# Performance work log

Measured on AMD Instinct MI355X. Metric: run time of the kernel, lower is better.

Reference implementation:

```python
import jax, jax.numpy as jnp
import numpy as np

B, C, H, W = 4, 64, 64, 64
C8 = C // 8

def setup_inputs() -> dict:
    key = jax.random.key(0)
    ks = jax.random.split(key, 7)
    s = 0.05
    x  = jax.random.normal(ks[0], (B, C, H, W), dtype=jnp.float32)
    wq = jax.random.normal(ks[1], (C8, C), dtype=jnp.float32) * s
    bq = jax.random.normal(ks[2], (C8,), dtype=jnp.float32) * s
    wk = jax.random.normal(ks[3], (C8, C), dtype=jnp.float32) * s
    bk = jax.random.normal(ks[4], (C8,), dtype=jnp.float32) * s
    wv = jax.random.normal(ks[5], (C, C), dtype=jnp.float32) * s
    bv = jax.random.normal(ks[6], (C,), dtype=jnp.float32) * s
    return {"x": x, "wq": wq, "bq": bq, "wk": wk, "bk": bk, "wv": wv, "bv": bv}

def reference(x, wq, bq, wk, bk, wv, bv):
    b, c, h, w = x.shape
    n = h * w
    xf = x.reshape(b, c, n)                                   # [B,C,N]
    q = jnp.einsum('oc,bcn->bon', wq, xf) + bq[None, :, None]  # [B,C8,N]
    k = jnp.einsum('oc,bcn->bon', wk, xf) + bk[None, :, None]  # [B,C8,N]
    v = jnp.einsum('oc,bcn->bon', wv, xf) + bv[None, :, None]  # [B,C, N]
    scores = jnp.einsum('bci,bcj->bij', q, k)                  # [B,N,N]
    attn = jax.nn.softmax(scores, axis=-1)
    out = jnp.einsum('bcn,bnm->bcm', v, attn)                  # V @ A, as torch.bmm(value, attention)
    return out.reshape(b, c, h, w) + x
```

## Files before the change

### kernel.cpp

```cpp
#include <hip/hip_runtime.h>
#include <hip/hip_bf16.h>
#include <math.h>

#define NN 4096
#define CC 64

typedef float  f32x16 __attribute__((ext_vector_type(16)));
typedef short  bf16x8 __attribute__((ext_vector_type(8)));
typedef short  s16x4  __attribute__((ext_vector_type(4)));
typedef unsigned int u32x4 __attribute__((ext_vector_type(4)));

static __device__ __forceinline__ unsigned short f2bfu(float f) {
    __hip_bfloat16 h = __float2bfloat16(f);
    unsigned short s;
    __builtin_memcpy(&s, &h, 2);
    return s;
}
static __device__ __forceinline__ unsigned packbf(float lo, float hi) {
    return (unsigned)f2bfu(lo) | ((unsigned)f2bfu(hi) << 16);
}
static __device__ __forceinline__ f32x16 fzero16() {
    f32x16 z;
#pragma unroll
    for (int i = 0; i < 16; ++i) z[i] = 0.f;
    return z;
}
static __device__ __forceinline__ bf16x8 bzero8() {
    bf16x8 z;
#pragma unroll
    for (int i = 0; i < 8; ++i) z[i] = 0;
    return z;
}

static __device__ __forceinline__ void process_phalf(
        const f32x16& s, int hi,
        bf16x8 a0, bf16x8 a1, bf16x8 a2, bf16x8 a3,
        f32x16& accX, f32x16& accY) {
    unsigned g0 = packbf(__expf(s[0]),  __expf(s[1]));
    unsigned g1 = packbf(__expf(s[2]),  __expf(s[3]));
    unsigned g2 = packbf(__expf(s[4]),  __expf(s[5]));
    unsigned g3 = packbf(__expf(s[6]),  __expf(s[7]));
    unsigned g4 = packbf(__expf(s[8]),  __expf(s[9]));
    unsigned g5 = packbf(__expf(s[10]), __expf(s[11]));
    unsigned g6 = packbf(__expf(s[12]), __expf(s[13]));
    unsigned g7 = packbf(__expf(s[14]), __expf(s[15]));
    unsigned r0 = (unsigned)__shfl_xor((int)(hi ? g0 : g2), 32);
    unsigned r1 = (unsigned)__shfl_xor((int)(hi ? g1 : g3), 32);
    unsigned r2 = (unsigned)__shfl_xor((int)(hi ? g4 : g6), 32);
    unsigned r3 = (unsigned)__shfl_xor((int)(hi ? g5 : g7), 32);
    u32x4 b0u, b1u;
    b0u[0] = hi ? r0 : g0;  b0u[1] = hi ? r1 : g1;
    b0u[2] = hi ? g2 : r0;  b0u[3] = hi ? g3 : r1;
    b1u[0] = hi ? r2 : g4;  b1u[1] = hi ? r3 : g5;
    b1u[2] = hi ? g6 : r2;  b1u[3] = hi ? g7 : r3;
    bf16x8 bf0 = __builtin_bit_cast(bf16x8, b0u);
    bf16x8 bf1 = __builtin_bit_cast(bf16x8, b1u);
    accX = __builtin_amdgcn_mfma_f32_32x32x16_bf16(a0, bf0, accX, 0, 0, 0);
    accX = __builtin_amdgcn_mfma_f32_32x32x16_bf16(a1, bf1, accX, 0, 0, 0);
    accY = __builtin_amdgcn_mfma_f32_32x32x16_bf16(a2, bf0, accY, 0, 0, 0);
    accY = __builtin_amdgcn_mfma_f32_32x32x16_bf16(a3, bf1, accY, 0, 0, 0);
}

__global__ __launch_bounds__(256) void proj_all(
        const float* __restrict__ x,
        const float* __restrict__ wq, const float* __restrict__ bq,
        const float* __restrict__ wk, const float* __restrict__ bk,
        const float* __restrict__ wv, const float* __restrict__ bv,
        short* __restrict__ qb, short* __restrict__ kb, float* __restrict__ vT) {
    int t = threadIdx.x;
    int w = t >> 6, ml = t & 31, hi = (t >> 5) & 1;
    int rt = blockIdx.x >> 7;
    int nt = (blockIdx.x & 127) * 4 + w;
    int ng = nt * 32 + ml;
    int b = ng >> 12, nb_ = ng & 4095;
    const float* xc = x + ((size_t)b * CC) * NN + nb_;

    int rg = 32 * rt + ml;
    const float* wrow =
        rg < 8  ? wq + (size_t)rg * 64 :
        rg < 16 ? wk + (size_t)(rg - 8) * 64 :
        rg < 80 ? wv + (size_t)(rg - 16) * 64 : wq;
    bool wvalid = (rg < 80);

    f32x16 acc = fzero16();
#pragma unroll
    for (int s = 0; s < 4; ++s) {
        int c0 = 16 * s + 8 * hi;
        float xv[8];
#pragma unroll
        for (int j = 0; j < 8; ++j) xv[j] = xc[(size_t)(c0 + j) * NN];
        u32x4 xg;
#pragma unroll
        for (int j = 0; j < 4; ++j) xg[j] = packbf(xv[2 * j], xv[2 * j + 1]);
        bf16x8 xf = __builtin_bit_cast(bf16x8, xg);

        bf16x8 af;
        if (wvalid) {
            float4 f0 = *(const float4*)(wrow + c0);
            float4 f1 = *(const float4*)(wrow + c0 + 4);
            u32x4 ag;
            ag[0] = packbf(f0.x, f0.y); ag[1] = packbf(f0.z, f0.w);
            ag[2] = packbf(f1.x, f1.y); ag[3] = packbf(f1.z, f1.w);
            af = __builtin_bit_cast(bf16x8, ag);
        } else {
            af = bzero8();
        }
        acc = __builtin_amdgcn_mfma_f32_32x32x16_bf16(af, xf, acc, 0, 0, 0);
    }

    if (rt == 0) {
        s16x4 qv, kv;
#pragma unroll
        for (int j = 0; j < 4; ++j) {
            qv[j] = (short)f2bfu(acc[j] + bq[j + 4 * hi]);
            kv[j] = (short)f2bfu(acc[j + 4] + bk[j + 4 * hi]);
        }
        *(s16x4*)(qb + (size_t)ng * 8 + 4 * hi) = qv;
        *(s16x4*)(kb + (size_t)ng * 8 + 4 * hi) = kv;
#pragma unroll
        for (int r = 8; r < 16; ++r) {
            int rowr = (r & 3) + 8 * (r >> 2) + 4 * hi;
            int c = rowr - 16;
            vT[((size_t)(b * CC + c)) * NN + nb_] = acc[r] + bv[c];
        }
    } else if (rt == 1) {
#pragma unroll
        for (int r = 0; r < 16; ++r) {
            int rowr = (r & 3) + 8 * (r >> 2) + 4 * hi;
            int c = rowr + 16;
            vT[((size_t)(b * CC + c)) * NN + nb_] = acc[r] + bv[c];
        }
    } else {
#pragma unroll
        for (int r = 0; r < 8; ++r) {
            int rowr = (r & 3) + 8 * (r >> 2) + 4 * hi;
            int c = rowr + 48;
            vT[((size_t)(b * CC + c)) * NN + nb_] = acc[r] + bv[c];
        }
    }
}

__global__ __launch_bounds__(512) void stats_mfma(
        const short* __restrict__ qb, const short* __restrict__ kb,
        const float* __restrict__ vT, short* __restrict__ vsT) {
    int b = blockIdx.x >> 7;
    int nbase = (blockIdx.x & 127) * 32;
    int t = threadIdx.x;
    int w = __builtin_amdgcn_readfirstlane(t >> 6);
    int ml = t & 31, hi = (t >> 5) & 1;

    bf16x8 qf = bzero8();
    if (!hi) qf = *(const bf16x8*)(qb + ((size_t)(b * NN + nbase + ml)) * 8);
    const short* kbb = kb + ((size_t)b * NN) * 8;

    float accl[16];
#pragma unroll
    for (int r = 0; r < 16; ++r) accl[r] = 0.f;

    bf16x8 kf0 = bzero8();
    if (!hi) kf0 = *(const bf16x8*)(kbb + (size_t)(w * 32 + ml) * 8);

    for (int i = 0; i < 16; ++i) {
        int mchn = (i < 15) ? (w + 8 * (i + 1)) : w;
        bf16x8 kf1 = bzero8();
        if (!hi) kf1 = *(const bf16x8*)(kbb + (size_t)(mchn * 32 + ml) * 8);
        f32x16 s = __builtin_amdgcn_mfma_f32_32x32x16_bf16(qf, kf0, fzero16(), 0, 0, 0);
#pragma unroll
        for (int r = 0; r < 16; ++r) accl[r] += __expf(s[r]);
        kf0 = kf1;
    }

#pragma unroll
    for (int r = 0; r < 16; ++r) {
#pragma unroll
        for (int mask = 1; mask <= 16; mask <<= 1)
            accl[r] += __shfl_xor(accl[r], mask);
    }

    __shared__ float rs[32];
    if (t < 32) rs[t] = 0.f;
    __syncthreads();
    if (ml == 0) {
#pragma unroll
        for (int r = 0; r < 16; ++r) {
            int rowr = (r & 3) + 8 * (r >> 2) + 4 * hi;
            atomicAdd(&rs[rowr], accl[r]);
        }
    }
    __syncthreads();

    float inv = 1.0f / rs[t & 31];
    int nl = nbase + (t & 31);
#pragma unroll
    for (int cl = 0; cl < 4; ++cl) {
        int c = 16 * cl + (t >> 5);
        size_t idx = ((size_t)(b * CC + c)) * NN + nl;
        vsT[idx] = (short)f2bfu(vT[idx] * inv);
    }
}

__global__ __launch_bounds__(512, 2) void attn_pv(
        const short* __restrict__ qb, const short* __restrict__ kb,
        const short* __restrict__ vsT,
        const float* __restrict__ x, float* __restrict__ out) {
    __shared__ float red[4][64][68];

    int b = blockIdx.x >> 6;
    int mbase = (blockIdx.x & 63) << 6;
    int t = threadIdx.x;
    int w = __builtin_amdgcn_readfirstlane(t >> 6);
    int ml = t & 31, hi = (t >> 5) & 1;

    bf16x8 kf0 = bzero8(), kf1 = bzero8();
    if (!hi) {
        kf0 = *(const bf16x8*)(kb + ((size_t)(b * NN + mbase + ml)) * 8);
        kf1 = *(const bf16x8*)(kb + ((size_t)(b * NN + mbase + 32 + ml)) * 8);
    }

    f32x16 accA = fzero16(), accB = fzero16();
    f32x16 accC = fzero16(), accD = fzero16();

    const short* qbb = qb + ((size_t)b * NN) * 8;
    const short* v0p = vsT + ((size_t)(b * CC) + ml) * NN;
    const short* v1p = v0p + (size_t)32 * NN;

    int n0 = w * 32;
    bf16x8 qf_c = bzero8();
    if (!hi) qf_c = *(const bf16x8*)(qbb + (size_t)(n0 + ml) * 8);
    bf16x8 a00_p = *(const bf16x8*)(v0p + n0 + 8 * hi);
    bf16x8 a01_p = *(const bf16x8*)(v0p + n0 + 16 + 8 * hi);
    bf16x8 a10_p = *(const bf16x8*)(v1p + n0 + 8 * hi);
    bf16x8 a11_p = *(const bf16x8*)(v1p + n0 + 16 + 8 * hi);

    f32x16 s0p = __builtin_amdgcn_mfma_f32_32x32x16_bf16(qf_c, kf0, fzero16(), 0, 0, 0);
    f32x16 s1p = __builtin_amdgcn_mfma_f32_32x32x16_bf16(qf_c, kf1, fzero16(), 0, 0, 0);

    int n1 = (w + 8) * 32;
    if (!hi) qf_c = *(const bf16x8*)(qbb + (size_t)(n1 + ml) * 8);
    else     qf_c = bzero8();
    bf16x8 a00_c = *(const bf16x8*)(v0p + n1 + 8 * hi);
    bf16x8 a01_c = *(const bf16x8*)(v0p + n1 + 16 + 8 * hi);
    bf16x8 a10_c = *(const bf16x8*)(v1p + n1 + 8 * hi);
    bf16x8 a11_c = *(const bf16x8*)(v1p + n1 + 16 + 8 * hi);

    for (int j = 1; j < 16; ++j) {
        int nn = (j < 15) ? (w + 8 * (j + 1)) * 32 : w * 32;
        bf16x8 qf_n = bzero8();
        if (!hi) qf_n = *(const bf16x8*)(qbb + (size_t)(nn + ml) * 8);
        bf16x8 a00_n = *(const bf16x8*)(v0p + nn + 8 * hi);
        bf16x8 a01_n = *(const bf16x8*)(v0p + nn + 16 + 8 * hi);
        bf16x8 a10_n = *(const bf16x8*)(v1p + nn + 8 * hi);
        bf16x8 a11_n = *(const bf16x8*)(v1p + nn + 16 + 8 * hi);

        process_phalf(s0p, hi, a00_p, a01_p, a10_p, a11_p, accA, accC);
        process_phalf(s1p, hi, a00_p, a01_p, a10_p, a11_p, accB, accD);

        s0p = __builtin_amdgcn_mfma_f32_32x32x16_bf16(qf_c, kf0, fzero16(), 0, 0, 0);
        s1p = __builtin_amdgcn_mfma_f32_32x32x16_bf16(qf_c, kf1, fzero16(), 0, 0, 0);

        a00_p = a00_c; a01_p = a01_c; a10_p = a10_c; a11_p = a11_c;
        a00_c = a00_n; a01_c = a01_n; a10_c = a10_n; a11_c = a11_n;
        qf_c = qf_n;
    }
    process_phalf(s0p, hi, a00_p, a01_p, a10_p, a11_p, accA, accC);
    process_phalf(s1p, hi, a00_p, a01_p, a10_p, a11_p, accB, accD);

    int q4 = w & 3;
    if (w >= 4) {
#pragma unroll
        for (int r = 0; r < 16; ++r) {
            int rowr = (r & 3) + 8 * (r >> 2) + 4 * hi;
            red[q4][rowr][ml]           = accA[r];
            red[q4][rowr][32 + ml]      = accB[r];
            red[q4][rowr + 32][ml]      = accC[r];
            red[q4][rowr + 32][32 + ml] = accD[r];
        }
    }
    __syncthreads();
    if (w < 4) {
#pragma unroll
        for (int r = 0; r < 16; ++r) {
            int rowr = (r & 3) + 8 * (r >> 2) + 4 * hi;
            red[q4][rowr][ml]           += accA[r];
            red[q4][rowr][32 + ml]      += accB[r];
            red[q4][rowr + 32][ml]      += accC[r];
            red[q4][rowr + 32][32 + ml] += accD[r];
        }
    }
    __syncthreads();

    int c = t >> 3;
    int m0 = (t & 7) << 3;
    float4 s0 = *(float4*)&red[0][c][m0];
    float4 s1 = *(float4*)&red[0][c][m0 + 4];
#pragma unroll
    for (int q = 1; q < 4; ++q) {
        float4 a = *(float4*)&red[q][c][m0];
        float4 b4 = *(float4*)&red[q][c][m0 + 4];
        s0.x += a.x; s0.y += a.y; s0.z += a.z; s0.w += a.w;
        s1.x += b4.x; s1.y += b4.y; s1.z += b4.z; s1.w += b4.w;
    }
    size_t idx = ((size_t)(b * CC + c)) * NN + mbase + m0;
    float4 xa = *(const float4*)(x + idx);
    float4 xb = *(const float4*)(x + idx + 4);
    s0.x += xa.x; s0.y += xa.y; s0.z += xa.z; s0.w += xa.w;
    s1.x += xb.x; s1.y += xb.y; s1.z += xb.z; s1.w += xb.w;
    *(float4*)(out + idx) = s0;
    *(float4*)(out + idx + 4) = s1;
}

extern "C" void kernel_launch(void* const* d_in, const int* in_sizes, int n_in,
                              void* d_out, int out_size, void* d_ws, size_t ws_size,
                              hipStream_t stream) {
    const float* x  = (const float*)d_in[0];
    const float* wq = (const float*)d_in[1];
    const float* bq = (const float*)d_in[2];
    const float* wk = (const float*)d_in[3];
    const float* bk = (const float*)d_in[4];
    const float* wv = (const float*)d_in[5];
    const float* bv = (const float*)d_in[6];
    float* out = (float*)d_out;

    char* ws = (char*)d_ws;
    short* qb  = (short*)(ws);
    short* kb  = (short*)(ws + (256u << 10));
    float* vT  = (float*)(ws + (512u << 10));
    short* vsT = (short*)(ws + (512u << 10) + (4u << 20));

    proj_all  <<<384, 256, 0, stream>>>(x, wq, bq, wk, bk, wv, bv, qb, kb, vT);
    stats_mfma<<<512, 512, 0, stream>>>(qb, kb, vT, vsT);
    attn_pv   <<<256, 512, 0, stream>>>(qb, kb, vsT, x, out);
}
```

Baseline: 46.17 us.

## Fold softmax row normalization into QK MFMA via augmented log-sum channels

Q and K rows are padded from 8 to 16 bf16 channels. The extra Q channels carry log(rowsum) as a hi/lo bf16 pair, and the matching K channels are -1, so the score MFMA yields s - log(sum) directly. The stats kernel now writes only that log value instead of rescaling and converting all of V, and the projection kernel writes V straight to bf16. This removes the fp32 vT round trip and the per-element V scaling pass. In exchange, the QK MFMA uses the full 16-wide K dimension, which doubles the Q/K storage and loads, and the hi/lo split of the log sum may introduce small precision error.

```diff
diff --git a/kernel.cpp b/kernel.cpp
--- a/kernel.cpp
+++ b/kernel.cpp
@@ -66,7 +66,7 @@
         const float* __restrict__ wq, const float* __restrict__ bq,
         const float* __restrict__ wk, const float* __restrict__ bk,
         const float* __restrict__ wv, const float* __restrict__ bv,
-        short* __restrict__ qb, short* __restrict__ kb, float* __restrict__ vT) {
+        short* __restrict__ qb, short* __restrict__ kb, short* __restrict__ vsT) {
     int t = threadIdx.x;
     int w = t >> 6, ml = t & 31, hi = (t >> 5) & 1;
     int rt = blockIdx.x >> 7;
@@ -115,34 +115,40 @@
             qv[j] = (short)f2bfu(acc[j] + bq[j + 4 * hi]);
             kv[j] = (short)f2bfu(acc[j + 4] + bk[j + 4 * hi]);
         }
-        *(s16x4*)(qb + (size_t)ng * 8 + 4 * hi) = qv;
-        *(s16x4*)(kb + (size_t)ng * 8 + 4 * hi) = kv;
+        *(s16x4*)(qb + (size_t)ng * 16 + 4 * hi) = qv;
+        *(s16x4*)(kb + (size_t)ng * 16 + 4 * hi) = kv;
+        s16x4 qaux, kaux;
+#pragma unroll
+        for (int j = 0; j < 4; ++j) { qaux[j] = 0; kaux[j] = 0; }
+        if (!hi) { kaux[0] = (short)f2bfu(-1.0f); kaux[1] = (short)f2bfu(-1.0f); }
+        *(s16x4*)(qb + (size_t)ng * 16 + 8 + 4 * hi) = qaux;
+        *(s16x4*)(kb + (size_t)ng * 16 + 8 + 4 * hi) = kaux;
 #pragma unroll
         for (int r = 8; r < 16; ++r) {
             int rowr = (r & 3) + 8 * (r >> 2) + 4 * hi;
             int c = rowr - 16;
-            vT[((size_t)(b * CC + c)) * NN + nb_] = acc[r] + bv[c];
+            vsT[((size_t)(b * CC + c)) * NN + nb_] = (short)f2bfu(acc[r] + bv[c]);
         }
     } else if (rt == 1) {
 #pragma unroll
         for (int r = 0; r < 16; ++r) {
             int rowr = (r & 3) + 8 * (r >> 2) + 4 * hi;
             int c = rowr + 16;
-            vT[((size_t)(b * CC + c)) * NN + nb_] = acc[r] + bv[c];
+            vsT[((size_t)(b * CC + c)) * NN + nb_] = (short)f2bfu(acc[r] + bv[c]);
         }
     } else {
 #pragma unroll
         for (int r = 0; r < 8; ++r) {
             int rowr = (r & 3) + 8 * (r >> 2) + 4 * hi;
             int c = rowr + 48;
-            vT[((size_t)(b * CC + c)) * NN + nb_] = acc[r] + bv[c];
+            vsT[((size_t)(b * CC + c)) * NN + nb_] = (short)f2bfu(acc[r] + bv[c]);
         }
     }
 }
 
 __global__ __launch_bounds__(512) void stats_mfma(
         const short* __restrict__ qb, const short* __restrict__ kb,
-        const float* __restrict__ vT, short* __restrict__ vsT) {
+        short* __restrict__ qb_out) {
     int b = blockIdx.x >> 7;
     int nbase = (blockIdx.x & 127) * 32;
     int t = threadIdx.x;
@@ -150,20 +156,20 @@
     int ml = t & 31, hi = (t >> 5) & 1;
 
     bf16x8 qf = bzero8();
-    if (!hi) qf = *(const bf16x8*)(qb + ((size_t)(b * NN + nbase + ml)) * 8);
-    const short* kbb = kb + ((size_t)b * NN) * 8;
+    if (!hi) qf = *(const bf16x8*)(qb + ((size_t)(b * NN + nbase + ml)) * 16);
+    const short* kbb = kb + ((size_t)b * NN) * 16;
 
     float accl[16];
 #pragma unroll
     for (int r = 0; r < 16; ++r) accl[r] = 0.f;
 
     bf16x8 kf0 = bzero8();
-    if (!hi) kf0 = *(const bf16x8*)(kbb + (size_t)(w * 32 + ml) * 8);
+    if (!hi) kf0 = *(const bf16x8*)(kbb + (size_t)(w * 32 + ml) * 16);
 
     for (int i = 0; i < 16; ++i) {
         int mchn = (i < 15) ? (w + 8 * (i + 1)) : w;
         bf16x8 kf1 = bzero8();
-        if (!hi) kf1 = *(const bf16x8*)(kbb + (size_t)(mchn * 32 + ml) * 8);
+        if (!hi) kf1 = *(const bf16x8*)(kbb + (size_t)(mchn * 32 + ml) * 16);
         f32x16 s = __builtin_amdgcn_mfma_f32_32x32x16_bf16(qf, kf0, fzero16(), 0, 0, 0);
 #pragma unroll
         for (int r = 0; r < 16; ++r) accl[r] += __expf(s[r]);
@@ -189,13 +195,13 @@
     }
     __syncthreads();
 
-    float inv = 1.0f / rs[t & 31];
-    int nl = nbase + (t & 31);
-#pragma unroll
-    for (int cl = 0; cl < 4; ++cl) {
-        int c = 16 * cl + (t >> 5);
-        size_t idx = ((size_t)(b * CC + c)) * NN + nl;
-        vsT[idx] = (short)f2bfu(vT[idx] * inv);
+    if (t < 32) {
+        float ls = logf(rs[t]);
+        unsigned short h = f2bfu(ls);
+        float lhf = __builtin_bit_cast(float, ((unsigned)h) << 16);
+        unsigned short l2 = f2bfu(ls - lhf);
+        unsigned pk = (unsigned)h | ((unsigned)l2 << 16);
+        *(unsigned*)(qb_out + ((size_t)(b * NN + nbase + t)) * 16 + 8) = pk;
     }
 }
 
@@ -211,22 +217,18 @@
     int w = __builtin_amdgcn_readfirstlane(t >> 6);
     int ml = t & 31, hi = (t >> 5) & 1;
 
-    bf16x8 kf0 = bzero8(), kf1 = bzero8();
-    if (!hi) {
-        kf0 = *(const bf16x8*)(kb + ((size_t)(b * NN + mbase + ml)) * 8);
-        kf1 = *(const bf16x8*)(kb + ((size_t)(b * NN + mbase + 32 + ml)) * 8);
-    }
+    bf16x8 kf0 = *(const bf16x8*)(kb + ((size_t)(b * NN + mbase + ml)) * 16 + 8 * hi);
+    bf16x8 kf1 = *(const bf16x8*)(kb + ((size_t)(b * NN + mbase + 32 + ml)) * 16 + 8 * hi);
 
     f32x16 accA = fzero16(), accB = fzero16();
     f32x16 accC = fzero16(), accD = fzero16();
 
-    const short* qbb = qb + ((size_t)b * NN) * 8;
+    const short* qbb = qb + ((size_t)b * NN) * 16;
     const short* v0p = vsT + ((size_t)(b * CC) + ml) * NN;
     const short* v1p = v0p + (size_t)32 * NN;
 
     int n0 = w * 32;
-    bf16x8 qf_c = bzero8();
-    if (!hi) qf_c = *(const bf16x8*)(qbb + (size_t)(n0 + ml) * 8);
+    bf16x8 qf_c = *(const bf16x8*)(qbb + (size_t)(n0 + ml) * 16 + 8 * hi);
     bf16x8 a00_p = *(const bf16x8*)(v0p + n0 + 8 * hi);
     bf16x8 a01_p = *(const bf16x8*)(v0p + n0 + 16 + 8 * hi);
     bf16x8 a10_p = *(const bf16x8*)(v1p + n0 + 8 * hi);
@@ -236,8 +238,7 @@
     f32x16 s1p = __builtin_amdgcn_mfma_f32_32x32x16_bf16(qf_c, kf1, fzero16(), 0, 0, 0);
 
     int n1 = (w + 8) * 32;
-    if (!hi) qf_c = *(const bf16x8*)(qbb + (size_t)(n1 + ml) * 8);
-    else     qf_c = bzero8();
+    qf_c = *(const bf16x8*)(qbb + (size_t)(n1 + ml) * 16 + 8 * hi);
     bf16x8 a00_c = *(const bf16x8*)(v0p + n1 + 8 * hi);
     bf16x8 a01_c = *(const bf16x8*)(v0p + n1 + 16 + 8 * hi);
     bf16x8 a10_c = *(const bf16x8*)(v1p + n1 + 8 * hi);
@@ -245,8 +246,7 @@
 
     for (int j = 1; j < 16; ++j) {
         int nn = (j < 15) ? (w + 8 * (j + 1)) * 32 : w * 32;
-        bf16x8 qf_n = bzero8();
-        if (!hi) qf_n = *(const bf16x8*)(qbb + (size_t)(nn + ml) * 8);
+        bf16x8 qf_n = *(const bf16x8*)(qbb + (size_t)(nn + ml) * 16 + 8 * hi);
         bf16x8 a00_n = *(const bf16x8*)(v0p + nn + 8 * hi);
         bf16x8 a01_n = *(const bf16x8*)(v0p + nn + 16 + 8 * hi);
         bf16x8 a10_n = *(const bf16x8*)(v1p + nn + 8 * hi);
@@ -323,11 +323,10 @@
 
     char* ws = (char*)d_ws;
     short* qb  = (short*)(ws);
-    short* kb  = (short*)(ws + (256u << 10));
-    float* vT  = (float*)(ws + (512u << 10));
-    short* vsT = (short*)(ws + (512u << 10) + (4u << 20));
-
-    proj_all  <<<384, 256, 0, stream>>>(x, wq, bq, wk, bk, wv, bv, qb, kb, vT);
-    stats_mfma<<<512, 512, 0, stream>>>(qb, kb, vT, vsT);
+    short* kb  = (short*)(ws + (512u << 10));
+    short* vsT = (short*)(ws + (1u << 20));
+
+    proj_all  <<<384, 256, 0, stream>>>(x, wq, bq, wk, bk, wv, bv, qb, kb, vsT);
+    stats_mfma<<<512, 512, 0, stream>>>(qb, kb, qb);
     attn_pv   <<<256, 512, 0, stream>>>(qb, kb, vsT, x, out);
 }
```

Result: slower. 47.47 us (+2.8%).
